# Kernel optimization log

Measured on AMD Instinct MI355X. Metric: run time of the kernel, lower is better.

Reference implementation:

```python
import jax, jax.numpy as jnp
import numpy as np

EMB, BS, H = 512, 1024, 8
HD = EMB // H
B, L = 8, 1024
EPS = 1e-5

def setup_inputs() -> dict:
    key = jax.random.key(0)
    ks = jax.random.split(key, 12)
    s = EMB ** -0.5
    return {
        "x": jax.random.normal(ks[0], (B, L, EMB), jnp.float32),
        "ln_g": jnp.ones((EMB,), jnp.float32),
        "ln_b": jnp.zeros((EMB,), jnp.float32),
        "Wq": jax.random.normal(ks[1], (EMB, EMB), jnp.float32) * s,
        "bq": jnp.zeros((EMB,), jnp.float32),
        "Wk": jax.random.normal(ks[2], (EMB, EMB), jnp.float32) * s,
        "bk": jnp.zeros((EMB,), jnp.float32),
        "Wv": jax.random.normal(ks[3], (EMB, EMB), jnp.float32) * s,
        "bv": jnp.zeros((EMB,), jnp.float32),
        "Wo": jax.random.normal(ks[4], (EMB, EMB), jnp.float32) * s,
        "bo": jnp.zeros((EMB,), jnp.float32),
        "Er": jax.random.normal(ks[5], (H, BS, HD), jnp.float32),
    }

def reference(x, ln_g, ln_b, Wq, bq, Wk, bk, Wv, bv, Wo, bo, Er):
    b, l, d = x.shape
    # LayerNorm
    mu = jnp.mean(x, axis=-1, keepdims=True)
    var = jnp.mean((x - mu) ** 2, axis=-1, keepdims=True)
    h = (x - mu) * jax.lax.rsqrt(var + EPS) * ln_g + ln_b
    # projections -> (B, H, L, HD)
    def split_heads(t):
        return t.reshape(b, l, H, HD).transpose(0, 2, 1, 3)
    q = split_heads(h @ Wq + bq)
    k = split_heads(h @ Wk + bk)
    v = split_heads(h @ Wv + bv)
    scores = jnp.einsum('bhld,bhkd->bhlk', q, k) * (HD ** -0.5)
    # relative bias: QEr_all[b,h,l,r] = q . Er[h,r]; then gather r = (k - l) mod BS
    QEr_all = jnp.einsum('bhld,hrd->bhlr', q, Er)  # (B,H,L,BS)
    rel = (jnp.arange(l)[None, :] - jnp.arange(l)[:, None]) % BS  # (L,L), torch negative-index wrap
    QEr = jnp.take_along_axis(QEr_all, rel[None, None], axis=-1)  # (B,H,L,L)
    w = jax.nn.softmax(scores + QEr, axis=-1)
    out = jnp.einsum('bhlk,bhkd->bhld', w, v)
    out = out.transpose(0, 2, 1, 3).reshape(b, l, d)
    return out @ Wo + bo
```

## Files before the change

### kernel.cpp

```cpp
#include <hip/hip_runtime.h>
#include <hip/hip_bf16.h>


typedef __bf16 bf16;
typedef __bf16 bf16x8 __attribute__((ext_vector_type(8)));
typedef float floatx4 __attribute__((ext_vector_type(4)));
typedef float f32x4 __attribute__((ext_vector_type(4)));

#define MFMA16 __builtin_amdgcn_mfma_f32_16x16x32_bf16

#define KS 72
#define BSS 83
#define PSS 72
#define GS 40
#define TS 72

__global__ __launch_bounds__(256) void prep_ln_kernel(
    const float* __restrict__ Wq, const float* __restrict__ Wk,
    const float* __restrict__ Wv, const float* __restrict__ Wo,
    const float* __restrict__ Er,
    const float* __restrict__ x, const float* __restrict__ g,
    const float* __restrict__ bvec,
    bf16* __restrict__ wt, bf16* __restrict__ er_b, bf16* __restrict__ h) {
  __shared__ __align__(16) bf16 T[64 * TS];
  int blk = blockIdx.x;
  int tid = threadIdx.x;
  if (blk < 256) {
    int w = blk >> 6, rem = blk & 63;
    int r0 = (rem >> 3) << 6, c0 = (rem & 7) << 6;
    const float* W = (w == 0) ? Wq : (w == 1) ? Wk : (w == 2) ? Wv : Wo;
    int row = tid >> 2, cc = (tid & 3) << 4;
    const f32x4* src = (const f32x4*)(W + (r0 + row) * 512 + c0 + cc);
#pragma unroll
    for (int q2 = 0; q2 < 4; q2++) {
      f32x4 v = src[q2];
#pragma unroll
      for (int j = 0; j < 4; j++)
        T[(cc + q2 * 4 + j) * TS + row] = (bf16)v[j];
    }
    __syncthreads();
    int nloc = tid >> 2, kc = (tid & 3) << 4;
    bf16x8 a = *(const bf16x8*)(T + nloc * TS + kc);
    bf16x8 b = *(const bf16x8*)(T + nloc * TS + kc + 8);
    bf16* dst = wt + (w << 18) + (c0 + nloc) * 512 + r0 + kc;
    *(bf16x8*)dst = a;
    *(bf16x8*)(dst + 8) = b;
    return;
  }
  if (blk < 2304) {
    int e = (blk - 256) * 256 + tid;
    er_b[e] = (bf16)Er[e];
    return;
  }
  int row = (blk - 2304) * 4 + (tid >> 6);
  int lane = tid & 63;
  const f32x4* xr = (const f32x4*)(x + row * 512 + lane * 8);
  f32x4 v0 = xr[0], v1 = xr[1];
  float f[8] = {v0[0], v0[1], v0[2], v0[3], v1[0], v1[1], v1[2], v1[3]};
  float s = 0.f, ss = 0.f;
#pragma unroll
  for (int i = 0; i < 8; i++) { s += f[i]; ss += f[i] * f[i]; }
#pragma unroll
  for (int m = 1; m < 64; m <<= 1) { s += __shfl_xor(s, m); ss += __shfl_xor(ss, m); }
  float mean = s * (1.0f / 512.0f);
  float var = ss * (1.0f / 512.0f) - mean * mean;
  float inv = rsqrtf(var + 1e-5f);
  const f32x4* gr = (const f32x4*)(g + lane * 8);
  const f32x4* br = (const f32x4*)(bvec + lane * 8);
  f32x4 g0 = gr[0], g1 = gr[1], b0 = br[0], b1 = br[1];
  float gg[8] = {g0[0], g0[1], g0[2], g0[3], g1[0], g1[1], g1[2], g1[3]};
  float bb[8] = {b0[0], b0[1], b0[2], b0[3], b1[0], b1[1], b1[2], b1[3]};
  bf16x8 o;
#pragma unroll
  for (int i = 0; i < 8; i++)
    o[i] = (bf16)((f[i] - mean) * inv * gg[i] + bb[i]);
  *(bf16x8*)(h + row * 512 + lane * 8) = o;
}


__global__ __launch_bounds__(256) void qkv_gemm(
    const bf16* __restrict__ A,
    const bf16* __restrict__ wt,
    const float* __restrict__ bq, const float* __restrict__ bk,
    const float* __restrict__ bv,
    bf16* __restrict__ q_ws, bf16* __restrict__ k_ws, bf16* __restrict__ vt_ws) {
  __shared__ __align__(16) bf16 smem[64 * 264];
  bf16* As = smem;
  bf16* Bs = smem + 128 * GS;
  int m0 = blockIdx.x * 128;
  int ng0 = blockIdx.y * 128;
  int w = ng0 >> 9;
  int n0 = ng0 & 511;
  const bf16* Bt = wt + (w << 18);
  int tid = threadIdx.x;
  int wave = tid >> 6, lane = tid & 63, quad = lane >> 4, l16 = lane & 15;
  int mq = (wave >> 1) * 64, nq = (wave & 1) * 64;

  floatx4 acc[4][4] = {};
  for (int k0 = 0; k0 < 512; k0 += 32) {
    int r = tid >> 1, c = (tid & 1) * 16;
    *(bf16x8*)(As + r * GS + c)     = *(const bf16x8*)(A + (m0 + r) * 512 + k0 + c);
    *(bf16x8*)(As + r * GS + c + 8) = *(const bf16x8*)(A + (m0 + r) * 512 + k0 + c + 8);
    *(bf16x8*)(Bs + r * GS + c)     = *(const bf16x8*)(Bt + (n0 + r) * 512 + k0 + c);
    *(bf16x8*)(Bs + r * GS + c + 8) = *(const bf16x8*)(Bt + (n0 + r) * 512 + k0 + c + 8);
    __syncthreads();
    bf16x8 a[4], b[4];
#pragma unroll
    for (int mt = 0; mt < 4; mt++)
      a[mt] = *(const bf16x8*)(As + (mq + mt * 16 + l16) * GS + quad * 8);
#pragma unroll
    for (int nt = 0; nt < 4; nt++)
      b[nt] = *(const bf16x8*)(Bs + (nq + nt * 16 + l16) * GS + quad * 8);
#pragma unroll
    for (int mt = 0; mt < 4; mt++)
#pragma unroll
      for (int nt = 0; nt < 4; nt++)
        acc[mt][nt] = MFMA16(a[mt], b[nt], acc[mt][nt], 0, 0, 0);
    __syncthreads();
  }

  if (w == 2) {
#pragma unroll
    for (int nt = 0; nt < 4; nt++) {
      int col = n0 + nq + nt * 16 + l16;
      float bb = bv[col];
      int d = col & 63;
#pragma unroll
      for (int mt = 0; mt < 4; mt++)
#pragma unroll
        for (int r = 0; r < 4; r++) {
          int lloc = mq + mt * 16 + quad * 4 + r;
          smem[d * 264 + (wave & 1) * 128 + lloc] = (bf16)(acc[mt][nt][r] + bb);
        }
    }
    __syncthreads();
    int b_ = m0 >> 10, l0g = m0 & 1023;
    int dloc = tid >> 4, lc = (tid & 15) * 8;
#pragma unroll
    for (int h2 = 0; h2 < 2; h2++) {
      int bh = b_ * 8 + ((n0 + h2 * 64) >> 6);
#pragma unroll
      for (int dd = 0; dd < 4; dd++) {
        int d = dd * 16 + dloc;
        bf16x8 v = *(const bf16x8*)(smem + d * 264 + h2 * 128 + lc);
        *(bf16x8*)(vt_ws + (bh << 16) + (d << 10) + l0g + lc) = v;
      }
    }
    return;
  }

  const float* bias = (w == 0) ? bq : bk;
#pragma unroll
  for (int nt = 0; nt < 4; nt++) {
    int col = n0 + nq + nt * 16 + l16;
    float bb = bias[col];
    int hh = col >> 6, d = col & 63;
#pragma unroll
    for (int mt = 0; mt < 4; mt++) {
#pragma unroll
      for (int r = 0; r < 4; r++) {
        int mrow = m0 + mq + mt * 16 + quad * 4 + r;
        int b_ = mrow >> 10, l = mrow & 1023;
        int bh = b_ * 8 + hh;
        float v = acc[mt][nt][r] + bb;
        if (w == 0) q_ws[(bh << 16) + (l << 6) + d] = (bf16)v;
        else        k_ws[(bh << 16) + (l << 6) + d] = (bf16)(v * 0.125f);
      }
    }
  }
}

__global__ __launch_bounds__(256, 2) void attn_kernel(
    const bf16* __restrict__ q_ws, const bf16* __restrict__ k_ws,
    const bf16* __restrict__ vt_ws, const bf16* __restrict__ Er,
    bf16* __restrict__ o_ws) {
  __shared__ __align__(16) bf16 Ks_s[64 * KS];
  __shared__ __align__(16) bf16 Vs[64 * KS];
  __shared__ __align__(16) bf16 Ers[192 * KS];
  __shared__ __align__(16) float bias_s[4][16 * BSS];
  __shared__ __align__(16) bf16 Ps[4][16 * PSS];

  int qt = blockIdx.x;
  int bh = blockIdx.y;
  int hh = bh & 7;
  int l0 = qt << 7;
  int tid = threadIdx.x, wave = tid >> 6, lane = tid & 63;
  int quad = lane >> 4, l16 = lane & 15;

  bf16x8 aq0[2], aq1[2];
#pragma unroll
  for (int strip = 0; strip < 2; strip++) {
    const bf16* qb = q_ws + (bh << 16) + ((l0 + strip * 64 + wave * 16 + l16) << 6);
    aq0[strip] = *(const bf16x8*)(qb + quad * 8);
    aq1[strip] = *(const bf16x8*)(qb + 32 + quad * 8);
  }

  const bf16* kbh = k_ws + (bh << 16);
  const bf16* vbh = vt_ws + (bh << 16);
  const bf16* ebh = Er + (hh << 16);
  float* bw = bias_s[wave];
  bf16* pw = Ps[wave];

  float l_run[2][4] = {};
  floatx4 acc_o[2][4] = {};

  int e0 = -l0 - 127 + 2048;
#pragma unroll
  for (int i = 0; i < 4; i++) {
    int o = tid + i * 256;
    int row = o >> 3, ch = (o & 7) * 8;
    int grow = (e0 + row) & 1023;
    *(bf16x8*)(Ers + row * KS + ch) = *(const bf16x8*)(ebh + (grow << 6) + ch);
  }
  int sb = 0;

  for (int kt = 0; kt < 16; kt++) {
    int k0 = kt * 64;
#pragma unroll
    for (int i = 0; i < 2; i++) {
      int o = tid + i * 256;
      int row = o >> 3, ch = (o & 7) * 8;
      *(bf16x8*)(Ks_s + row * KS + ch) =
          *(const bf16x8*)(kbh + ((k0 + row) << 6) + ch);
      *(bf16x8*)(Vs + row * KS + ch) =
          *(const bf16x8*)(vbh + (row << 10) + k0 + ch);
    }
    {
      int s8 = sb + 8; if (s8 >= 12) s8 -= 12;
      int srow0 = s8 << 4;
#pragma unroll
      for (int i = 0; i < 2; i++) {
        int o = tid + i * 256;
        int row = o >> 3, ch = (o & 7) * 8;
        int grow = (e0 + 128 + k0 + row) & 1023;
        *(bf16x8*)(Ers + (srow0 + row) * KS + ch) =
            *(const bf16x8*)(ebh + (grow << 6) + ch);
      }
    }
    __syncthreads();

    bf16x8 kb0[4], kb1[4], vb0[4], vb1[4];
#pragma unroll
    for (int nt = 0; nt < 4; nt++) {
      const bf16* kr = Ks_s + (nt * 16 + l16) * KS + quad * 8;
      kb0[nt] = *(const bf16x8*)kr;
      kb1[nt] = *(const bf16x8*)(kr + 32);
      const bf16* vr = Vs + (nt * 16 + l16) * KS + quad * 8;
      vb0[nt] = *(const bf16x8*)vr;
      vb1[nt] = *(const bf16x8*)(vr + 32);
    }

#pragma unroll
    for (int strip = 0; strip < 2; strip++) {
      floatx4 acc_s[4] = {};
#pragma unroll
      for (int nt = 0; nt < 4; nt++) {
        acc_s[nt] = MFMA16(aq0[strip], kb0[nt], acc_s[nt], 0, 0, 0);
        acc_s[nt] = MFMA16(aq1[strip], kb1[nt], acc_s[nt], 0, 0, 0);
      }
      int t0 = (strip ? 3 : 7) - wave;
#pragma unroll
      for (int nt2 = 0; nt2 < 5; nt2++) {
        int tt = sb + t0 + nt2; if (tt >= 12) tt -= 12;
        const bf16* er = Ers + ((tt << 4) + l16) * KS + quad * 8;
        bf16x8 b0 = *(const bf16x8*)er;
        bf16x8 b1 = *(const bf16x8*)(er + 32);
        floatx4 accb = {};
        accb = MFMA16(aq0[strip], b0, accb, 0, 0, 0);
        accb = MFMA16(aq1[strip], b1, accb, 0, 0, 0);
#pragma unroll
        for (int r = 0; r < 4; r++)
          bw[(quad * 4 + r) * BSS + nt2 * 16 + l16] = accb[r];
      }
      float pv[4][4];
#pragma unroll
      for (int nt = 0; nt < 4; nt++) {
        int dk = nt * 16 + l16;
#pragma unroll
        for (int r = 0; r < 4; r++) {
          int sdl = quad * 4 + r;
          float sc = acc_s[nt][r] + bw[sdl * BSS + 15 + dk - sdl];
          pv[nt][r] = __expf(sc);
        }
      }
#pragma unroll
      for (int r = 0; r < 4; r++)
        l_run[strip][r] += pv[0][r] + pv[1][r] + pv[2][r] + pv[3][r];
#pragma unroll
      for (int nt = 0; nt < 4; nt++)
#pragma unroll
        for (int r = 0; r < 4; r++)
          pw[(quad * 4 + r) * PSS + nt * 16 + l16] = (bf16)pv[nt][r];
      bf16x8 ap0 = *(const bf16x8*)(pw + l16 * PSS + quad * 8);
      bf16x8 ap1 = *(const bf16x8*)(pw + l16 * PSS + 32 + quad * 8);
#pragma unroll
      for (int dt = 0; dt < 4; dt++) {
        acc_o[strip][dt] = MFMA16(ap0, vb0[dt], acc_o[strip][dt], 0, 0, 0);
        acc_o[strip][dt] = MFMA16(ap1, vb1[dt], acc_o[strip][dt], 0, 0, 0);
      }
    }
    sb += 4; if (sb >= 12) sb -= 12;
    __syncthreads();
  }

#pragma unroll
  for (int strip = 0; strip < 2; strip++) {
    float invl[4];
#pragma unroll
    for (int r = 0; r < 4; r++) {
      float lr = l_run[strip][r];
#pragma unroll
      for (int m = 1; m < 16; m <<= 1) lr += __shfl_xor(lr, m);
      invl[r] = 1.0f / lr;
    }
#pragma unroll
    for (int dt = 0; dt < 4; dt++) {
      int col = (hh << 6) + dt * 16 + l16;
#pragma unroll
      for (int r = 0; r < 4; r++) {
        int row = ((bh >> 3) << 10) + l0 + strip * 64 + wave * 16 + quad * 4 + r;
        o_ws[row * 512 + col] = (bf16)(acc_o[strip][dt][r] * invl[r]);
      }
    }
  }
}

__global__ __launch_bounds__(256) void out_gemm(
    const bf16* __restrict__ A,
    const bf16* __restrict__ Bt,
    const float* __restrict__ bo, float* __restrict__ out) {
  __shared__ __align__(16) bf16 As[128 * GS];
  __shared__ __align__(16) bf16 Bs[128 * GS];
  int m0 = blockIdx.x * 128;
  int n0 = blockIdx.y * 128;
  int tid = threadIdx.x;
  int wave = tid >> 6, lane = tid & 63, quad = lane >> 4, l16 = lane & 15;
  int mq = (wave >> 1) * 64, nq = (wave & 1) * 64;

  floatx4 acc[4][4] = {};
  for (int k0 = 0; k0 < 512; k0 += 32) {
    int r = tid >> 1, c = (tid & 1) * 16;
    *(bf16x8*)(As + r * GS + c)     = *(const bf16x8*)(A + (m0 + r) * 512 + k0 + c);
    *(bf16x8*)(As + r * GS + c + 8) = *(const bf16x8*)(A + (m0 + r) * 512 + k0 + c + 8);
    *(bf16x8*)(Bs + r * GS + c)     = *(const bf16x8*)(Bt + (n0 + r) * 512 + k0 + c);
    *(bf16x8*)(Bs + r * GS + c + 8) = *(const bf16x8*)(Bt + (n0 + r) * 512 + k0 + c + 8);
    __syncthreads();
    bf16x8 a[4], b[4];
#pragma unroll
    for (int mt = 0; mt < 4; mt++)
      a[mt] = *(const bf16x8*)(As + (mq + mt * 16 + l16) * GS + quad * 8);
#pragma unroll
    for (int nt = 0; nt < 4; nt++)
      b[nt] = *(const bf16x8*)(Bs + (nq + nt * 16 + l16) * GS + quad * 8);
#pragma unroll
    for (int mt = 0; mt < 4; mt++)
#pragma unroll
      for (int nt = 0; nt < 4; nt++)
        acc[mt][nt] = MFMA16(a[mt], b[nt], acc[mt][nt], 0, 0, 0);
    __syncthreads();
  }
#pragma unroll
  for (int nt = 0; nt < 4; nt++) {
    int col = n0 + nq + nt * 16 + l16;
    float bb = bo[col];
#pragma unroll
    for (int mt = 0; mt < 4; mt++) {
#pragma unroll
      for (int r = 0; r < 4; r++) {
        int mrow = m0 + mq + mt * 16 + quad * 4 + r;
        out[mrow * 512 + col] = acc[mt][nt][r] + bb;
      }
    }
  }
}

extern "C" void kernel_launch(void* const* d_in, const int* in_sizes, int n_in,
                              void* d_out, int out_size, void* d_ws, size_t ws_size,
                              hipStream_t stream) {
  const float* x    = (const float*)d_in[0];
  const float* ln_g = (const float*)d_in[1];
  const float* ln_b = (const float*)d_in[2];
  const float* Wq   = (const float*)d_in[3];
  const float* bq   = (const float*)d_in[4];
  const float* Wk   = (const float*)d_in[5];
  const float* bk   = (const float*)d_in[6];
  const float* Wv   = (const float*)d_in[7];
  const float* bv   = (const float*)d_in[8];
  const float* Wo   = (const float*)d_in[9];
  const float* bo   = (const float*)d_in[10];
  const float* Er   = (const float*)d_in[11];
  float* out = (float*)d_out;

  char* ws = (char*)d_ws;
  bf16* wt    = (bf16*)(ws);
  bf16* er_b  = (bf16*)(ws + (2u << 20));
  bf16* h     = (bf16*)(ws + (3u << 20));
  bf16* o_ws  = h;
  bf16* q_ws  = (bf16*)(ws + (11u << 20));
  bf16* k_ws  = (bf16*)(ws + (19u << 20));
  bf16* vt_ws = (bf16*)(ws + (27u << 20));

  prep_ln_kernel<<<4352, 256, 0, stream>>>(Wq, Wk, Wv, Wo, Er, x, ln_g, ln_b,
                                           wt, er_b, h);
  qkv_gemm<<<dim3(64, 12), 256, 0, stream>>>(h, wt, bq, bk, bv, q_ws, k_ws, vt_ws);
  attn_kernel<<<dim3(8, 64), 256, 0, stream>>>(q_ws, k_ws, vt_ws, er_b, o_ws);
  out_gemm<<<dim3(64, 4), 256, 0, stream>>>(o_ws, wt + 3 * 262144, bo, out);
}
```

Baseline: 201.3 us.

## Replace LDS bias scratch with cross-lane shuffles and register-cached Er tiles

```diff
diff --git a/kernel.cpp b/kernel.cpp
--- a/kernel.cpp
+++ b/kernel.cpp
@@ -10,7 +10,6 @@
 #define MFMA16 __builtin_amdgcn_mfma_f32_16x16x32_bf16
 
 #define KS 72
-#define BSS 83
 #define PSS 72
 #define GS 40
 #define TS 72
@@ -177,7 +176,6 @@
   __shared__ __align__(16) bf16 Ks_s[64 * KS];
   __shared__ __align__(16) bf16 Vs[64 * KS];
   __shared__ __align__(16) bf16 Ers[192 * KS];
-  __shared__ __align__(16) float bias_s[4][16 * BSS];
   __shared__ __align__(16) bf16 Ps[4][16 * PSS];
 
   int qt = blockIdx.x;
@@ -198,7 +196,6 @@
   const bf16* kbh = k_ws + (bh << 16);
   const bf16* vbh = vt_ws + (bh << 16);
   const bf16* ebh = Er + (hh << 16);
-  float* bw = bias_s[wave];
   bf16* pw = Ps[wave];
 
   float l_run[2][4] = {};
@@ -211,6 +208,15 @@
     int row = o >> 3, ch = (o & 7) * 8;
     int grow = (e0 + row) & 1023;
     *(bf16x8*)(Ers + row * KS + ch) = *(const bf16x8*)(ebh + (grow << 6) + ch);
+  }
+  __syncthreads();
+  bf16x8 ec0[5], ec1[5];
+#pragma unroll
+  for (int i = 0; i < 5; i++) {
+    int tt = 3 - wave + i;
+    const bf16* er = Ers + ((tt << 4) + l16) * KS + quad * 8;
+    ec0[i] = *(const bf16x8*)er;
+    ec1[i] = *(const bf16x8*)(er + 32);
   }
   int sb = 0;
 
@@ -251,36 +257,45 @@
     }
 
 #pragma unroll
-    for (int strip = 0; strip < 2; strip++) {
+    for (int pass = 0; pass < 2; pass++) {
+      int strip = 1 - pass;
       floatx4 acc_s[4] = {};
 #pragma unroll
       for (int nt = 0; nt < 4; nt++) {
         acc_s[nt] = MFMA16(aq0[strip], kb0[nt], acc_s[nt], 0, 0, 0);
         acc_s[nt] = MFMA16(aq1[strip], kb1[nt], acc_s[nt], 0, 0, 0);
       }
-      int t0 = (strip ? 3 : 7) - wave;
-#pragma unroll
-      for (int nt2 = 0; nt2 < 5; nt2++) {
-        int tt = sb + t0 + nt2; if (tt >= 12) tt -= 12;
-        const bf16* er = Ers + ((tt << 4) + l16) * KS + quad * 8;
-        bf16x8 b0 = *(const bf16x8*)er;
-        bf16x8 b1 = *(const bf16x8*)(er + 32);
-        floatx4 accb = {};
-        accb = MFMA16(aq0[strip], b0, accb, 0, 0, 0);
-        accb = MFMA16(aq1[strip], b1, accb, 0, 0, 0);
-#pragma unroll
-        for (int r = 0; r < 4; r++)
-          bw[(quad * 4 + r) * BSS + nt2 * 16 + l16] = accb[r];
+      floatx4 accb[5];
+#pragma unroll
+      for (int t = 0; t < 5; t++) {
+        floatx4 a = {};
+        a = MFMA16(aq0[strip], ec0[t], a, 0, 0, 0);
+        a = MFMA16(aq1[strip], ec1[t], a, 0, 0, 0);
+        accb[t] = a;
+      }
+      if (pass == 0) {
+#pragma unroll
+        for (int i = 0; i < 5; i++) {
+          int tt = sb + 7 - wave + i; if (tt >= 12) tt -= 12;
+          const bf16* er = Ers + ((tt << 4) + l16) * KS + quad * 8;
+          ec0[i] = *(const bf16x8*)er;
+          ec1[i] = *(const bf16x8*)(er + 32);
+        }
       }
       float pv[4][4];
 #pragma unroll
-      for (int nt = 0; nt < 4; nt++) {
-        int dk = nt * 16 + l16;
-#pragma unroll
-        for (int r = 0; r < 4; r++) {
-          int sdl = quad * 4 + r;
-          float sc = acc_s[nt][r] + bw[sdl * BSS + 15 + dk - sdl];
-          pv[nt][r] = __expf(sc);
+      for (int r = 0; r < 4; r++) {
+        int sdl = quad * 4 + r;
+        int dd = l16 - sdl;
+        int cc = (dd <= 0) ? (15 + dd) : (dd - 1);
+        int src = (quad << 4) | cc;
+        float rot[5];
+#pragma unroll
+        for (int t = 0; t < 5; t++) rot[t] = __shfl(accb[t][r], src);
+#pragma unroll
+        for (int nt = 0; nt < 4; nt++) {
+          float b = (dd > 0) ? rot[nt + 1] : rot[nt];
+          pv[nt][r] = __expf(acc_s[nt][r] + b);
         }
       }
 #pragma unroll
```

After: 191.6 us. 1.05x faster.

## Double-buffer K/V in LDS, register-prefetch Er, shuffle relative bias instead of LDS

Applied to the files above, without the earlier changes.

```diff
diff --git a/kernel.cpp b/kernel.cpp
--- a/kernel.cpp
+++ b/kernel.cpp
@@ -10,10 +10,10 @@
 #define MFMA16 __builtin_amdgcn_mfma_f32_16x16x32_bf16
 
 #define KS 72
-#define BSS 83
 #define PSS 72
 #define GS 40
 #define TS 72
+#define UNRL _Pragma("unroll")
 
 __global__ __launch_bounds__(256) void prep_ln_kernel(
     const float* __restrict__ Wq, const float* __restrict__ Wk,
@@ -170,14 +170,106 @@
   }
 }
 
+#define SOFTMAX_PV(S)                                                         \
+      float pv4[4][4];                                                        \
+      UNRL for (int r = 0; r < 4; r++) {                                      \
+        int sdl = quad * 4 + r;                                               \
+        int cc = (l16 <= sdl) ? (15 + l16 - sdl) : (l16 - sdl - 1);           \
+        int src = (quad << 4) | cc;                                           \
+        bool hi = (l16 >= 15 - sdl);                                          \
+        UNRL for (int nt = 0; nt < 4; nt++) {                                 \
+          float sel = hi ? accb[nt][r] : accb[nt + 1][r];                     \
+          float b = __shfl(sel, src);                                         \
+          pv4[nt][r] = __expf(acc_s[nt][r] + b);                              \
+        }                                                                     \
+      }                                                                       \
+      UNRL for (int r = 0; r < 4; r++)                                        \
+        l_run[S][r] += pv4[0][r] + pv4[1][r] + pv4[2][r] + pv4[3][r];         \
+      UNRL for (int nt = 0; nt < 4; nt++)                                     \
+        UNRL for (int r = 0; r < 4; r++)                                      \
+          pw[(quad * 4 + r) * PSS + nt * 16 + l16] = (bf16)pv4[nt][r];        \
+      {                                                                       \
+        bf16x8 ap0 = *(const bf16x8*)(pw + l16 * PSS + quad * 8);             \
+        bf16x8 ap1 = *(const bf16x8*)(pw + l16 * PSS + 32 + quad * 8);        \
+        UNRL for (int dt = 0; dt < 4; dt++) {                                 \
+          acc_o[S][dt] = MFMA16(ap0, vb0[dt], acc_o[S][dt], 0, 0, 0);         \
+          acc_o[S][dt] = MFMA16(ap1, vb1[dt], acc_o[S][dt], 0, 0, 0);         \
+        }                                                                     \
+      }
+
+#define ATTN_STEP(KT, BSEL, E10, E11, E00, E01)                               \
+  {                                                                           \
+    bf16* Kb = Ks_s[BSEL];                                                    \
+    bf16* Vb = Vs[BSEL];                                                      \
+    *(bf16x8*)(Kb + sr0 * KS + sc0) = pk[0];                                  \
+    *(bf16x8*)(Kb + sr1 * KS + sc0) = pk[1];                                  \
+    *(bf16x8*)(Vb + sr0 * KS + sc0) = pvv[0];                                 \
+    *(bf16x8*)(Vb + sr1 * KS + sc0) = pvv[1];                                 \
+    __syncthreads();                                                          \
+    bf16x8 vb0[4], vb1[4];                                                    \
+    UNRL for (int nt = 0; nt < 4; nt++) {                                     \
+      const bf16* vr = Vb + (nt * 16 + l16) * KS + quad * 8;                  \
+      vb0[nt] = *(const bf16x8*)vr;                                           \
+      vb1[nt] = *(const bf16x8*)(vr + 32);                                    \
+    }                                                                         \
+    {                                                                         \
+      int kn0 = (((KT) + 1) & 15) * 64;                                       \
+      pk[0]  = *(const bf16x8*)(kbh + ((kn0 + sr0) << 6) + sc0);              \
+      pk[1]  = *(const bf16x8*)(kbh + ((kn0 + sr1) << 6) + sc0);              \
+      pvv[0] = *(const bf16x8*)(vbh + (sr0 << 10) + kn0 + sc0);               \
+      pvv[1] = *(const bf16x8*)(vbh + (sr1 << 10) + kn0 + sc0);               \
+    }                                                                         \
+    {                                                  \
+      floatx4 acc_s[4] = {};                                                  \
+      UNRL for (int nt = 0; nt < 4; nt++) {                                   \
+        const bf16* kr = Kb + (nt * 16 + l16) * KS + quad * 8;                \
+        bf16x8 kb0 = *(const bf16x8*)kr;                                      \
+        bf16x8 kb1 = *(const bf16x8*)(kr + 32);                               \
+        acc_s[nt] = MFMA16(aq0[1], kb0, acc_s[nt], 0, 0, 0);                  \
+        acc_s[nt] = MFMA16(aq1[1], kb1, acc_s[nt], 0, 0, 0);                  \
+      }                                                                       \
+      floatx4 accb[5];                                                        \
+      UNRL for (int t = 0; t < 5; t++) {                                      \
+        floatx4 a = {};                                                       \
+        a = MFMA16(aq0[1], E10[t], a, 0, 0, 0);                               \
+        a = MFMA16(aq1[1], E11[t], a, 0, 0, 0);                               \
+        accb[t] = a;                                                          \
+      }                                                                       \
+      UNRL for (int i = 0; i < 5; i++) {              \
+        int Tt = 4 * (KT) + 11 - wave + i;                                    \
+        int grow = (e0 + Tt * 16 + l16) & 1023;                               \
+        const bf16* er = ebh + (grow << 6) + quad * 8;                        \
+        E10[i] = *(const bf16x8*)er;                                          \
+        E11[i] = *(const bf16x8*)(er + 32);                                   \
+      }                                                                       \
+      SOFTMAX_PV(1)                                                           \
+    }                                                                         \
+    {                                                  \
+      floatx4 acc_s[4] = {};                                                  \
+      UNRL for (int nt = 0; nt < 4; nt++) {                                   \
+        const bf16* kr = Kb + (nt * 16 + l16) * KS + quad * 8;                \
+        bf16x8 kb0 = *(const bf16x8*)kr;                                      \
+        bf16x8 kb1 = *(const bf16x8*)(kr + 32);                               \
+        acc_s[nt] = MFMA16(aq0[0], kb0, acc_s[nt], 0, 0, 0);                  \
+        acc_s[nt] = MFMA16(aq1[0], kb1, acc_s[nt], 0, 0, 0);                  \
+      }                                                                       \
+      floatx4 accb[5];                                                        \
+      UNRL for (int t = 0; t < 5; t++) {                                      \
+        floatx4 a = {};                                                       \
+        a = MFMA16(aq0[0], E00[t], a, 0, 0, 0);                               \
+        a = MFMA16(aq1[0], E01[t], a, 0, 0, 0);                               \
+        accb[t] = a;                                                          \
+      }                                                                       \
+      SOFTMAX_PV(0)                                                           \
+    }                                                                         \
+  }
+
 __global__ __launch_bounds__(256, 2) void attn_kernel(
     const bf16* __restrict__ q_ws, const bf16* __restrict__ k_ws,
     const bf16* __restrict__ vt_ws, const bf16* __restrict__ Er,
     bf16* __restrict__ o_ws) {
-  __shared__ __align__(16) bf16 Ks_s[64 * KS];
-  __shared__ __align__(16) bf16 Vs[64 * KS];
-  __shared__ __align__(16) bf16 Ers[192 * KS];
-  __shared__ __align__(16) float bias_s[4][16 * BSS];
+  __shared__ __align__(16) bf16 Ks_s[2][64 * KS];
+  __shared__ __align__(16) bf16 Vs[2][64 * KS];
   __shared__ __align__(16) bf16 Ps[4][16 * PSS];
 
   int qt = blockIdx.x;
@@ -198,109 +290,38 @@
   const bf16* kbh = k_ws + (bh << 16);
   const bf16* vbh = vt_ws + (bh << 16);
   const bf16* ebh = Er + (hh << 16);
-  float* bw = bias_s[wave];
   bf16* pw = Ps[wave];
 
   float l_run[2][4] = {};
   floatx4 acc_o[2][4] = {};
 
   int e0 = -l0 - 127 + 2048;
-#pragma unroll
-  for (int i = 0; i < 4; i++) {
-    int o = tid + i * 256;
-    int row = o >> 3, ch = (o & 7) * 8;
-    int grow = (e0 + row) & 1023;
-    *(bf16x8*)(Ers + row * KS + ch) = *(const bf16x8*)(ebh + (grow << 6) + ch);
-  }
-  int sb = 0;
-
-  for (int kt = 0; kt < 16; kt++) {
-    int k0 = kt * 64;
-#pragma unroll
-    for (int i = 0; i < 2; i++) {
-      int o = tid + i * 256;
-      int row = o >> 3, ch = (o & 7) * 8;
-      *(bf16x8*)(Ks_s + row * KS + ch) =
-          *(const bf16x8*)(kbh + ((k0 + row) << 6) + ch);
-      *(bf16x8*)(Vs + row * KS + ch) =
-          *(const bf16x8*)(vbh + (row << 10) + k0 + ch);
-    }
-    {
-      int s8 = sb + 8; if (s8 >= 12) s8 -= 12;
-      int srow0 = s8 << 4;
-#pragma unroll
-      for (int i = 0; i < 2; i++) {
-        int o = tid + i * 256;
-        int row = o >> 3, ch = (o & 7) * 8;
-        int grow = (e0 + 128 + k0 + row) & 1023;
-        *(bf16x8*)(Ers + (srow0 + row) * KS + ch) =
-            *(const bf16x8*)(ebh + (grow << 6) + ch);
-      }
-    }
-    __syncthreads();
-
-    bf16x8 kb0[4], kb1[4], vb0[4], vb1[4];
-#pragma unroll
-    for (int nt = 0; nt < 4; nt++) {
-      const bf16* kr = Ks_s + (nt * 16 + l16) * KS + quad * 8;
-      kb0[nt] = *(const bf16x8*)kr;
-      kb1[nt] = *(const bf16x8*)(kr + 32);
-      const bf16* vr = Vs + (nt * 16 + l16) * KS + quad * 8;
-      vb0[nt] = *(const bf16x8*)vr;
-      vb1[nt] = *(const bf16x8*)(vr + 32);
-    }
-
-#pragma unroll
-    for (int strip = 0; strip < 2; strip++) {
-      floatx4 acc_s[4] = {};
-#pragma unroll
-      for (int nt = 0; nt < 4; nt++) {
-        acc_s[nt] = MFMA16(aq0[strip], kb0[nt], acc_s[nt], 0, 0, 0);
-        acc_s[nt] = MFMA16(aq1[strip], kb1[nt], acc_s[nt], 0, 0, 0);
-      }
-      int t0 = (strip ? 3 : 7) - wave;
-#pragma unroll
-      for (int nt2 = 0; nt2 < 5; nt2++) {
-        int tt = sb + t0 + nt2; if (tt >= 12) tt -= 12;
-        const bf16* er = Ers + ((tt << 4) + l16) * KS + quad * 8;
-        bf16x8 b0 = *(const bf16x8*)er;
-        bf16x8 b1 = *(const bf16x8*)(er + 32);
-        floatx4 accb = {};
-        accb = MFMA16(aq0[strip], b0, accb, 0, 0, 0);
-        accb = MFMA16(aq1[strip], b1, accb, 0, 0, 0);
-#pragma unroll
-        for (int r = 0; r < 4; r++)
-          bw[(quad * 4 + r) * BSS + nt2 * 16 + l16] = accb[r];
-      }
-      float pv[4][4];
-#pragma unroll
-      for (int nt = 0; nt < 4; nt++) {
-        int dk = nt * 16 + l16;
-#pragma unroll
-        for (int r = 0; r < 4; r++) {
-          int sdl = quad * 4 + r;
-          float sc = acc_s[nt][r] + bw[sdl * BSS + 15 + dk - sdl];
-          pv[nt][r] = __expf(sc);
-        }
-      }
-#pragma unroll
-      for (int r = 0; r < 4; r++)
-        l_run[strip][r] += pv[0][r] + pv[1][r] + pv[2][r] + pv[3][r];
-#pragma unroll
-      for (int nt = 0; nt < 4; nt++)
-#pragma unroll
-        for (int r = 0; r < 4; r++)
-          pw[(quad * 4 + r) * PSS + nt * 16 + l16] = (bf16)pv[nt][r];
-      bf16x8 ap0 = *(const bf16x8*)(pw + l16 * PSS + quad * 8);
-      bf16x8 ap1 = *(const bf16x8*)(pw + l16 * PSS + 32 + quad * 8);
-#pragma unroll
-      for (int dt = 0; dt < 4; dt++) {
-        acc_o[strip][dt] = MFMA16(ap0, vb0[dt], acc_o[strip][dt], 0, 0, 0);
-        acc_o[strip][dt] = MFMA16(ap1, vb1[dt], acc_o[strip][dt], 0, 0, 0);
-      }
-    }
-    sb += 4; if (sb >= 12) sb -= 12;
-    __syncthreads();
+  bf16x8 eP0[5], eP1[5], eQ0[5], eQ1[5];
+#pragma unroll
+  for (int i = 0; i < 5; i++) {
+    int Tp = 3 - wave + i;
+    int gp = (e0 + Tp * 16 + l16) & 1023;
+    const bf16* ep = ebh + (gp << 6) + quad * 8;
+    eP0[i] = *(const bf16x8*)ep;
+    eP1[i] = *(const bf16x8*)(ep + 32);
+    int Tq = 7 - wave + i;
+    int gq = (e0 + Tq * 16 + l16) & 1023;
+    const bf16* eq = ebh + (gq << 6) + quad * 8;
+    eQ0[i] = *(const bf16x8*)eq;
+    eQ1[i] = *(const bf16x8*)(eq + 32);
+  }
+
+  int sr0 = tid >> 3, sc0 = (tid & 7) * 8;
+  int sr1 = sr0 + 32;
+  bf16x8 pk[2], pvv[2];
+  pk[0]  = *(const bf16x8*)(kbh + (sr0 << 6) + sc0);
+  pk[1]  = *(const bf16x8*)(kbh + (sr1 << 6) + sc0);
+  pvv[0] = *(const bf16x8*)(vbh + (sr0 << 10) + sc0);
+  pvv[1] = *(const bf16x8*)(vbh + (sr1 << 10) + sc0);
+
+  for (int kt2 = 0; kt2 < 16; kt2 += 2) {
+    ATTN_STEP(kt2,     0, eP0, eP1, eQ0, eQ1)
+    ATTN_STEP(kt2 + 1, 1, eQ0, eQ1, eP0, eP1)
   }
 
 #pragma unroll
```

Measured after the change: 219.3 us. 8.9% more time.
